# Kernel tuning notes

Hardware: AMD Instinct MI355X
Metric: run time of the kernel (lower is better)

## Reference

```python
import jax, jax.numpy as jnp
import numpy as np
from jax import lax

NUM_POINT = 2048   # S: number of FPS-sampled centers
RADIUS = 0.2       # ball-query radius
NUM_SAMPLE = 32    # K: neighbors per center


def setup_inputs() -> dict:
    key = jax.random.key(0)
    k1, k2 = jax.random.split(key)
    B, N, C = 4, 8192, 64
    xyz = jax.random.normal(k1, (B, N, 3), dtype=jnp.float32)
    features = jax.random.normal(k2, (B, C, N), dtype=jnp.float32)
    return {"xyz": xyz, "features": features}


def fps(xyz, npoint):
    """D-FPS (farthest point sampling on coords). xyz (B,N,3) -> idx (B,npoint) int32.
    Matches CUDA FPS: start at index 0, iteratively pick argmax of min-dist."""
    B, N, _ = xyz.shape

    def body(carry, _):
        min_d, last = carry
        p = jnp.take_along_axis(xyz, last[:, None, None], axis=1)  # (B,1,3)
        d = jnp.sum((xyz - p) ** 2, axis=-1)                        # (B,N)
        min_d = jnp.minimum(min_d, d)
        nxt = jnp.argmax(min_d, axis=-1).astype(jnp.int32)
        return (min_d, nxt), nxt

    idx0 = jnp.zeros((B,), jnp.int32)
    min_d0 = jnp.full((B, N), 1e10, dtype=xyz.dtype)
    (_, _), rest = lax.scan(body, (min_d0, idx0), None, length=npoint - 1)
    return jnp.concatenate([idx0[None], rest], axis=0).T  # (B, npoint)


def ball_query(radius, nsample, xyz, new_xyz):
    """For each center pick the first nsample point indices (in original order)
    with squared dist < radius^2; pad short lists with the first hit (0 if none).
    xyz (B,N,3), new_xyz (B,S,3) -> idx (B,S,nsample) int32."""
    N = xyz.shape[1]
    d2 = jnp.sum((new_xyz[:, :, None, :] - xyz[:, None, :, :]) ** 2, axis=-1)  # (B,S,N)
    mask = d2 < radius * radius
    # key = point index where in-ball, else N; nsample smallest keys = first hits in order
    key = jnp.where(mask, jnp.arange(N, dtype=jnp.int32)[None, None, :], N)
    _, idx = lax.top_k(-key, nsample)            # (B,S,nsample)
    idx = idx.astype(jnp.int32)
    valid = jnp.take_along_axis(mask, idx, axis=-1)
    first = jnp.where(valid[:, :, :1], idx[:, :, :1], 0)
    return jnp.where(valid, idx, first)


def reference(xyz, features):
    B, N, _ = xyz.shape
    C = features.shape[1]
    fps_idx = fps(xyz, NUM_POINT)                                       # (B,S)
    new_xyz = jnp.take_along_axis(xyz, fps_idx[:, :, None], axis=1)     # (B,S,3)
    idx = ball_query(RADIUS, NUM_SAMPLE, xyz, new_xyz)                  # (B,S,K)
    # grouped xyz, recentered on each sampled point
    grouped_xyz = jnp.take_along_axis(xyz[:, None], idx[..., None], axis=2)  # (B,S,K,3)
    grouped_xyz = grouped_xyz - new_xyz[:, :, None, :]
    # grouped features
    f = jnp.swapaxes(features, 1, 2)                                    # (B,N,C)
    grouped_f = jnp.take_along_axis(f[:, None], idx[..., None], axis=2)  # (B,S,K,C)
    # use_xyz=True: concat relative coords with features -> (B, 3+C, S, K)
    grouped = jnp.concatenate([grouped_xyz, grouped_f], axis=-1).transpose(0, 3, 1, 2)
    return (new_xyz, grouped, fps_idx)
```

## Files before the change

kernel.cpp:

```cpp
#include <hip/hip_runtime.h>

#define NPTS 8192
#define SPTS 2048
#define KS 32
#define CF 64
#define BQ 4
#define FPS_T 512
#define PPT (NPTS / FPS_T)
#define PPT2 (PPT / 2)
#define FPS_SHIFT 9

#define OFF_GROUPED 24576
#define GROUPED_SZ  17563648
#define OFF_FPSIDX  (OFF_GROUPED + GROUPED_SZ)

typedef __attribute__((ext_vector_type(2))) float vf2;
typedef unsigned long long u64;

#define DPPMAXF(x, ctrl) do {                                                   \
    int _t = __builtin_amdgcn_mov_dpp(__float_as_int(x), (ctrl), 0xf, 0xf, true); \
    x = fmaxf((x), __int_as_float(_t));                                         \
} while (0)

#define DPPMAXU(x, ctrl) do {                                                   \
    unsigned _u = (unsigned)__builtin_amdgcn_mov_dpp((int)(x), (ctrl), 0xf, 0xf, true); \
    x = ((x) > _u) ? (x) : _u;                                                  \
} while (0)

__global__ __launch_bounds__(FPS_T)
void fps_kernel(const float* __restrict__ xyz, float* __restrict__ out)
{
#pragma clang fp contract(off)
    __shared__ float sx[NPTS], sy[NPTS], sz[NPTS];
    __shared__ u64 slots[2][8];
    const int b    = blockIdx.x;
    const int tid  = threadIdx.x;
    const int wv   = tid >> 6;
    const int lane = tid & 63;
    const float* xb = xyz + (size_t)b * (NPTS * 3);

    vf2 PX[PPT2], PY[PPT2], PZ[PPT2], MD[PPT2];
#pragma unroll
    for (int j = 0; j < PPT2; ++j) {
        const int p0 = tid + FPS_T * (2 * j);
        const int p1 = p0 + FPS_T;
        const float x0 = xb[p0 * 3 + 0], y0 = xb[p0 * 3 + 1], z0 = xb[p0 * 3 + 2];
        const float x1 = xb[p1 * 3 + 0], y1 = xb[p1 * 3 + 1], z1 = xb[p1 * 3 + 2];
        sx[p0] = x0; sy[p0] = y0; sz[p0] = z0;
        sx[p1] = x1; sy[p1] = y1; sz[p1] = z1;
        vf2 vx; vx.x = x0; vx.y = x1; PX[j] = vx;
        vf2 vy; vy.x = y0; vy.y = y1; PY[j] = vy;
        vf2 vz; vz.x = z0; vz.y = z1; PZ[j] = vz;
        vf2 vm; vm.x = 1e10f; vm.y = 1e10f; MD[j] = vm;
    }

    float* newxyz = out;
    float* fpsidx = out + OFF_FPSIDX;

    float qx = xb[0], qy = xb[1], qz = xb[2];
    if (tid == 0) {
        fpsidx[(size_t)b * SPTS + 0] = 0.0f;
        newxyz[(size_t)b * SPTS * 3 + 0] = qx;
        newxyz[(size_t)b * SPTS * 3 + 1] = qy;
        newxyz[(size_t)b * SPTS * 3 + 2] = qz;
    }

    for (int i = 1; i < SPTS; ++i) {
        vf2 qxx; qxx.x = qx; qxx.y = qx;
        vf2 qyy; qyy.x = qy; qyy.y = qy;
        vf2 qzz; qzz.x = qz; qzz.y = qz;

#pragma unroll
        for (int j = 0; j < PPT2; ++j) {
            const vf2 dx = PX[j] - qxx;
            const vf2 dy = PY[j] - qyy;
            const vf2 dz = PZ[j] - qzz;
            const vf2 d  = (dx * dx + dy * dy) + dz * dz;
            MD[j] = __builtin_elementwise_min(MD[j], d);
        }

        vf2 m0 = __builtin_elementwise_max(MD[0], MD[1]);
        vf2 m1 = __builtin_elementwise_max(MD[2], MD[3]);
        vf2 m2 = __builtin_elementwise_max(MD[4], MD[5]);
        vf2 m3 = __builtin_elementwise_max(MD[6], MD[7]);
        m0 = __builtin_elementwise_max(m0, m1);
        m2 = __builtin_elementwise_max(m2, m3);
        m0 = __builtin_elementwise_max(m0, m2);
        const float best = fmaxf(m0.x, m0.y);

        int bj = PPT - 1;
#pragma unroll
        for (int j = PPT - 2; j >= 0; --j) {
            const float v = (j & 1) ? MD[j >> 1].y : MD[j >> 1].x;
            if (v == best) bj = j;
        }
        const int bidx = tid + (bj << FPS_SHIFT);

        float wm = best;
        DPPMAXF(wm, 0x111);
        DPPMAXF(wm, 0x112);
        DPPMAXF(wm, 0x114);
        DPPMAXF(wm, 0x118);
        DPPMAXF(wm, 0x142);
        DPPMAXF(wm, 0x143);
        const float wavemax =
            __int_as_float(__builtin_amdgcn_readlane(__float_as_int(wm), 63));

        unsigned cand = (best == wavemax) ? (unsigned)(NPTS - 1 - bidx) : 0u;
        DPPMAXU(cand, 0x111);
        DPPMAXU(cand, 0x112);
        DPPMAXU(cand, 0x114);
        DPPMAXU(cand, 0x118);
        DPPMAXU(cand, 0x142);
        DPPMAXU(cand, 0x143);
        const unsigned candmax =
            (unsigned)__builtin_amdgcn_readlane((int)cand, 63);

        const u64 pk = ((u64)__float_as_uint(wavemax) << 32) | candmax;
        if (lane == 0) slots[i & 1][wv] = pk;
        __syncthreads();

        u64 g = slots[i & 1][0];
#pragma unroll
        for (int w = 1; w < 8; ++w) {
            const u64 s = slots[i & 1][w];
            if (s > g) g = s;
        }
        const int widx = (NPTS - 1) - (int)(unsigned)(g & 0xffffffffull);

        qx = sx[widx]; qy = sy[widx]; qz = sz[widx];

        if (tid == 0) {
            fpsidx[(size_t)b * SPTS + i] = (float)widx;
            const size_t o = ((size_t)b * SPTS + i) * 3;
            newxyz[o + 0] = qx; newxyz[o + 1] = qy; newxyz[o + 2] = qz;
        }
    }
}

__global__ __launch_bounds__(256)
void ballgroup_kernel(const float* __restrict__ xyz, const float* __restrict__ feat,
                      float* out)
{
#pragma clang fp contract(off)
    __shared__ int idxl[4][KS];
    const int tid    = threadIdx.x;
    const int wv     = tid >> 6;
    const int lane   = tid & 63;
    const int center = blockIdx.x * 4 + wv;
    const int b      = center >> 11;
    const int s      = center & (SPTS - 1);
    const float* xb  = xyz + (size_t)b * (NPTS * 3);
    const float* newxyz = out;
    const float cx = newxyz[(size_t)center * 3 + 0];
    const float cy = newxyz[(size_t)center * 3 + 1];
    const float cz = newxyz[(size_t)center * 3 + 2];

    if (lane == 0) idxl[wv][0] = 0;

    int cnt = 0;
    for (int nb = 0; nb < NPTS; nb += 64) {
        const int p = nb + lane;
        const float x = xb[p * 3 + 0];
        const float y = xb[p * 3 + 1];
        const float z = xb[p * 3 + 2];
        const float dx = cx - x, dy = cy - y, dz = cz - z;
        const float d2 = (dx * dx + dy * dy) + dz * dz;
        const bool in = (d2 <= 0.04f);
        const unsigned long long mk = __ballot(in);
        if (in) {
            const int pos = cnt + __popcll(mk & ((1ull << lane) - 1ull));
            if (pos < KS) idxl[wv][pos] = p;
        }
        cnt += (int)__popcll(mk);
        if (cnt >= KS) break;
    }
    const int cc = cnt < KS ? cnt : KS;

    int myidx = 0;
    if (lane < KS) {
        myidx = (lane < cc) ? idxl[wv][lane] : idxl[wv][0];
        idxl[wv][lane] = myidx;
    }

    float* grouped = out + OFF_GROUPED;
    const size_t chstride = (size_t)SPTS * KS;
    const size_t base67   = (size_t)b * 67 * chstride + (size_t)s * KS;

    if (lane < KS) {
        const float gx = xb[(size_t)myidx * 3 + 0] - cx;
        const float gy = xb[(size_t)myidx * 3 + 1] - cy;
        const float gz = xb[(size_t)myidx * 3 + 2] - cz;
        grouped[base67 + 0 * chstride + lane] = gx;
        grouped[base67 + 1 * chstride + lane] = gy;
        grouped[base67 + 2 * chstride + lane] = gz;
    }

    const int k    = lane & (KS - 1);
    const int half = lane >> 5;
    const int gi   = idxl[wv][k];
    const float* fb = feat + (size_t)b * CF * NPTS;
    const size_t obase = base67 + 3 * chstride + (size_t)k;
#pragma unroll 8
    for (int c0 = 0; c0 < 32; ++c0) {
        const int c = c0 * 2 + half;
        grouped[obase + (size_t)c * chstride] = fb[(size_t)c * NPTS + gi];
    }
}

extern "C" void kernel_launch(void* const* d_in, const int* in_sizes, int n_in,
                              void* d_out, int out_size, void* d_ws, size_t ws_size,
                              hipStream_t stream) {
    const float* xyz  = (const float*)d_in[0];
    const float* feat = (const float*)d_in[1];
    float* out = (float*)d_out;
    fps_kernel<<<dim3(BQ), dim3(FPS_T), 0, stream>>>(xyz, out);
    ballgroup_kernel<<<dim3((BQ * SPTS) / 4), dim3(256), 0, stream>>>(xyz, feat, out);
}
```

Before: 1.907 ms.

## Fuse FPS wave argmax into single 64-bit DPP reduction and buffer results in LDS

The FPS loop now packs each lane's max distance and inverted index into one 64-bit key and reduces it with a single DPP chain. Before, it ran a float max reduction, a readlane, and then a second index reduction. The per-lane argmax scan is replaced by an equality bitmask plus count-trailing-zeros, and the cross-wave slot read uses 128-bit LDS loads. Per-iteration global stores of the sampled point and index are buffered in LDS and written out together after the loop. The goal is to shorten the serial critical path of each of the 2047 iterations, at the cost of more LDS use and 64-bit compares per DPP step.

```diff
diff --git a/kernel.cpp b/kernel.cpp
--- a/kernel.cpp
+++ b/kernel.cpp
@@ -17,14 +17,14 @@
 typedef __attribute__((ext_vector_type(2))) float vf2;
 typedef unsigned long long u64;
 
-#define DPPMAXF(x, ctrl) do {                                                   \
-    int _t = __builtin_amdgcn_mov_dpp(__float_as_int(x), (ctrl), 0xf, 0xf, true); \
-    x = fmaxf((x), __int_as_float(_t));                                         \
-} while (0)
-
-#define DPPMAXU(x, ctrl) do {                                                   \
-    unsigned _u = (unsigned)__builtin_amdgcn_mov_dpp((int)(x), (ctrl), 0xf, 0xf, true); \
-    x = ((x) > _u) ? (x) : _u;                                                  \
+#define DPPSTEP64(pk, ctrl) do {                                                  \
+    const unsigned _lo = (unsigned)(pk), _hi = (unsigned)((pk) >> 32);            \
+    const unsigned _olo =                                                         \
+        (unsigned)__builtin_amdgcn_mov_dpp((int)_lo, (ctrl), 0xf, 0xf, true);     \
+    const unsigned _ohi =                                                         \
+        (unsigned)__builtin_amdgcn_mov_dpp((int)_hi, (ctrl), 0xf, 0xf, true);     \
+    const u64 _o = ((u64)_ohi << 32) | _olo;                                      \
+    (pk) = (_o > (pk)) ? _o : (pk);                                               \
 } while (0)
 
 __global__ __launch_bounds__(FPS_T)
@@ -32,7 +32,8 @@
 {
 #pragma clang fp contract(off)
     __shared__ float sx[NPTS], sy[NPTS], sz[NPTS];
-    __shared__ u64 slots[2][8];
+    __shared__ float4 rres[SPTS];
+    __shared__ __align__(16) u64 slots[2][8];
     const int b    = blockIdx.x;
     const int tid  = threadIdx.x;
     const int wv   = tid >> 6;
@@ -54,15 +55,10 @@
         vf2 vm; vm.x = 1e10f; vm.y = 1e10f; MD[j] = vm;
     }
 
-    float* newxyz = out;
-    float* fpsidx = out + OFF_FPSIDX;
-
     float qx = xb[0], qy = xb[1], qz = xb[2];
     if (tid == 0) {
-        fpsidx[(size_t)b * SPTS + 0] = 0.0f;
-        newxyz[(size_t)b * SPTS * 3 + 0] = qx;
-        newxyz[(size_t)b * SPTS * 3 + 1] = qy;
-        newxyz[(size_t)b * SPTS * 3 + 2] = qz;
+        float4 r; r.x = qx; r.y = qy; r.z = qz; r.w = 0.0f;
+        rres[0] = r;
     }
 
     for (int i = 1; i < SPTS; ++i) {
@@ -88,53 +84,59 @@
         m0 = __builtin_elementwise_max(m0, m2);
         const float best = fmaxf(m0.x, m0.y);
 
-        int bj = PPT - 1;
+        unsigned k0 = ((MD[0].x == best) ? 0x0001u : 0u) | ((MD[0].y == best) ? 0x0002u : 0u);
+        unsigned k1 = ((MD[1].x == best) ? 0x0004u : 0u) | ((MD[1].y == best) ? 0x0008u : 0u);
+        unsigned k2 = ((MD[2].x == best) ? 0x0010u : 0u) | ((MD[2].y == best) ? 0x0020u : 0u);
+        unsigned k3 = ((MD[3].x == best) ? 0x0040u : 0u) | ((MD[3].y == best) ? 0x0080u : 0u);
+        unsigned k4 = ((MD[4].x == best) ? 0x0100u : 0u) | ((MD[4].y == best) ? 0x0200u : 0u);
+        unsigned k5 = ((MD[5].x == best) ? 0x0400u : 0u) | ((MD[5].y == best) ? 0x0800u : 0u);
+        unsigned k6 = ((MD[6].x == best) ? 0x1000u : 0u) | ((MD[6].y == best) ? 0x2000u : 0u);
+        unsigned k7 = ((MD[7].x == best) ? 0x4000u : 0u) | ((MD[7].y == best) ? 0x8000u : 0u);
+        k0 |= k1; k2 |= k3; k4 |= k5; k6 |= k7;
+        k0 |= k2; k4 |= k6;
+        const int bj = __builtin_ctz(k0 | k4);
+        const int bidx = tid + (bj << FPS_SHIFT);
+
+        u64 pk = ((u64)__float_as_uint(best) << 32) | (unsigned)(NPTS - 1 - bidx);
+
+        DPPSTEP64(pk, 0x111);
+        DPPSTEP64(pk, 0x112);
+        DPPSTEP64(pk, 0x114);
+        DPPSTEP64(pk, 0x118);
+        DPPSTEP64(pk, 0x142);
+        DPPSTEP64(pk, 0x143);
+        if (lane == 63) slots[i & 1][wv] = pk;
+        __syncthreads();
+
+        const ulonglong2* sp = (const ulonglong2*)slots[i & 1];
+        const ulonglong2 p0 = sp[0], p1 = sp[1], p2 = sp[2], p3 = sp[3];
+        u64 a = p0.x > p0.y ? p0.x : p0.y;
+        u64 c = p1.x > p1.y ? p1.x : p1.y;
+        u64 d = p2.x > p2.y ? p2.x : p2.y;
+        u64 e = p3.x > p3.y ? p3.x : p3.y;
+        a = a > c ? a : c;
+        d = d > e ? d : e;
+        const u64 g = a > d ? a : d;
+        const int widx = (NPTS - 1) - (int)(unsigned)(g & 0xffffffffull);
+
+        qx = sx[widx]; qy = sy[widx]; qz = sz[widx];
+
+        if (tid == 0) {
+            float4 r; r.x = qx; r.y = qy; r.z = qz; r.w = (float)widx;
+            rres[i] = r;
+        }
+    }
+
+    __syncthreads();
+    float* newxyz = out;
+    float* fpsidx = out + OFF_FPSIDX;
 #pragma unroll
-        for (int j = PPT - 2; j >= 0; --j) {
-            const float v = (j & 1) ? MD[j >> 1].y : MD[j >> 1].x;
-            if (v == best) bj = j;
-        }
-        const int bidx = tid + (bj << FPS_SHIFT);
-
-        float wm = best;
-        DPPMAXF(wm, 0x111);
-        DPPMAXF(wm, 0x112);
-        DPPMAXF(wm, 0x114);
-        DPPMAXF(wm, 0x118);
-        DPPMAXF(wm, 0x142);
-        DPPMAXF(wm, 0x143);
-        const float wavemax =
-            __int_as_float(__builtin_amdgcn_readlane(__float_as_int(wm), 63));
-
-        unsigned cand = (best == wavemax) ? (unsigned)(NPTS - 1 - bidx) : 0u;
-        DPPMAXU(cand, 0x111);
-        DPPMAXU(cand, 0x112);
-        DPPMAXU(cand, 0x114);
-        DPPMAXU(cand, 0x118);
-        DPPMAXU(cand, 0x142);
-        DPPMAXU(cand, 0x143);
-        const unsigned candmax =
-            (unsigned)__builtin_amdgcn_readlane((int)cand, 63);
-
-        const u64 pk = ((u64)__float_as_uint(wavemax) << 32) | candmax;
-        if (lane == 0) slots[i & 1][wv] = pk;
-        __syncthreads();
-
-        u64 g = slots[i & 1][0];
-#pragma unroll
-        for (int w = 1; w < 8; ++w) {
-            const u64 s = slots[i & 1][w];
-            if (s > g) g = s;
-        }
-        const int widx = (NPTS - 1) - (int)(unsigned)(g & 0xffffffffull);
-
-        qx = sx[widx]; qy = sy[widx]; qz = sz[widx];
-
-        if (tid == 0) {
-            fpsidx[(size_t)b * SPTS + i] = (float)widx;
-            const size_t o = ((size_t)b * SPTS + i) * 3;
-            newxyz[o + 0] = qx; newxyz[o + 1] = qy; newxyz[o + 2] = qz;
-        }
+    for (int j = 0; j < 4; ++j) {
+        const int i = tid + (j << FPS_SHIFT);
+        const float4 r = rres[i];
+        fpsidx[(size_t)b * SPTS + i] = r.w;
+        const size_t o = ((size_t)b * SPTS + i) * 3;
+        newxyz[o + 0] = r.x; newxyz[o + 1] = r.y; newxyz[o + 2] = r.z;
     }
 }
 
```

After: 2.051 ms. +7.6%, slower.

## Halve FPS block size, buffer results in LDS, and streamline argmax reduction

Applied to the files above, without the earlier changes.

The FPS kernel now runs 256 threads with 32 points per thread instead of 512 with 16. This cuts the barrier to 4 waves and the cross-wave slot reduction to two 16-byte LDS reads. Per-iteration global stores of sampled indices and coordinates are buffered in an LDS array and written out cooperatively at the end. Other changes: the argmax index search uses a bitmask plus ctz, the separate readlane of the candidate is dropped by having lane 63 write the slot, and inline packed add/mul asm keeps the arithmetic unfused. More work per thread raises register pressure and per-iteration serial ALU work, in exchange for cheaper synchronisation.

```diff
diff --git a/kernel.cpp b/kernel.cpp
--- a/kernel.cpp
+++ b/kernel.cpp
@@ -5,10 +5,10 @@
 #define KS 32
 #define CF 64
 #define BQ 4
-#define FPS_T 512
-#define PPT (NPTS / FPS_T)
-#define PPT2 (PPT / 2)
-#define FPS_SHIFT 9
+#define FPS_T 256
+#define PPT 32
+#define NPAIR 16
+#define FPS_SHIFT 8
 
 #define OFF_GROUPED 24576
 #define GROUPED_SZ  17563648
@@ -16,6 +16,13 @@
 
 typedef __attribute__((ext_vector_type(2))) float vf2;
 typedef unsigned long long u64;
+
+static __device__ __forceinline__ vf2 pk_add(vf2 a, vf2 b) {
+    vf2 d; asm("v_pk_add_f32 %0, %1, %2" : "=v"(d) : "v"(a), "v"(b)); return d;
+}
+static __device__ __forceinline__ vf2 pk_mul(vf2 a, vf2 b) {
+    vf2 d; asm("v_pk_mul_f32 %0, %1, %2" : "=v"(d) : "v"(a), "v"(b)); return d;
+}
 
 #define DPPMAXF(x, ctrl) do {                                                   \
     int _t = __builtin_amdgcn_mov_dpp(__float_as_int(x), (ctrl), 0xf, 0xf, true); \
@@ -32,18 +39,19 @@
 {
 #pragma clang fp contract(off)
     __shared__ float sx[NPTS], sy[NPTS], sz[NPTS];
-    __shared__ u64 slots[2][8];
+    __shared__ float4 rres[SPTS];
+    __shared__ __align__(16) u64 slots[2][4];
     const int b    = blockIdx.x;
     const int tid  = threadIdx.x;
     const int wv   = tid >> 6;
     const int lane = tid & 63;
     const float* xb = xyz + (size_t)b * (NPTS * 3);
 
-    vf2 PX[PPT2], PY[PPT2], PZ[PPT2], MD[PPT2];
-#pragma unroll
-    for (int j = 0; j < PPT2; ++j) {
-        const int p0 = tid + FPS_T * (2 * j);
-        const int p1 = p0 + FPS_T;
+    vf2 PX[NPAIR], PY[NPAIR], PZ[NPAIR], MD[NPAIR];
+#pragma unroll
+    for (int j = 0; j < NPAIR; ++j) {
+        const int p0 = tid + 512 * j;
+        const int p1 = p0 + 256;
         const float x0 = xb[p0 * 3 + 0], y0 = xb[p0 * 3 + 1], z0 = xb[p0 * 3 + 2];
         const float x1 = xb[p1 * 3 + 0], y1 = xb[p1 * 3 + 1], z1 = xb[p1 * 3 + 2];
         sx[p0] = x0; sy[p0] = y0; sz[p0] = z0;
@@ -54,47 +62,46 @@
         vf2 vm; vm.x = 1e10f; vm.y = 1e10f; MD[j] = vm;
     }
 
-    float* newxyz = out;
-    float* fpsidx = out + OFF_FPSIDX;
-
     float qx = xb[0], qy = xb[1], qz = xb[2];
     if (tid == 0) {
-        fpsidx[(size_t)b * SPTS + 0] = 0.0f;
-        newxyz[(size_t)b * SPTS * 3 + 0] = qx;
-        newxyz[(size_t)b * SPTS * 3 + 1] = qy;
-        newxyz[(size_t)b * SPTS * 3 + 2] = qz;
+        float4 r; r.x = qx; r.y = qy; r.z = qz; r.w = 0.0f;
+        rres[0] = r;
     }
 
     for (int i = 1; i < SPTS; ++i) {
-        vf2 qxx; qxx.x = qx; qxx.y = qx;
-        vf2 qyy; qyy.x = qy; qyy.y = qy;
-        vf2 qzz; qzz.x = qz; qzz.y = qz;
-
-#pragma unroll
-        for (int j = 0; j < PPT2; ++j) {
-            const vf2 dx = PX[j] - qxx;
-            const vf2 dy = PY[j] - qyy;
-            const vf2 dz = PZ[j] - qzz;
-            const vf2 d  = (dx * dx + dy * dy) + dz * dz;
-            MD[j] = __builtin_elementwise_min(MD[j], d);
-        }
-
-        vf2 m0 = __builtin_elementwise_max(MD[0], MD[1]);
-        vf2 m1 = __builtin_elementwise_max(MD[2], MD[3]);
-        vf2 m2 = __builtin_elementwise_max(MD[4], MD[5]);
-        vf2 m3 = __builtin_elementwise_max(MD[6], MD[7]);
-        m0 = __builtin_elementwise_max(m0, m1);
-        m2 = __builtin_elementwise_max(m2, m3);
-        m0 = __builtin_elementwise_max(m0, m2);
-        const float best = fmaxf(m0.x, m0.y);
-
-        int bj = PPT - 1;
-#pragma unroll
-        for (int j = PPT - 2; j >= 0; --j) {
-            const float v = (j & 1) ? MD[j >> 1].y : MD[j >> 1].x;
-            if (v == best) bj = j;
-        }
-        const int bidx = tid + (bj << FPS_SHIFT);
+        const float nqx = -qx, nqy = -qy, nqz = -qz;
+        vf2 vnx; vnx.x = nqx; vnx.y = nqx;
+        vf2 vny; vny.x = nqy; vny.y = nqy;
+        vf2 vnz; vnz.x = nqz; vnz.y = nqz;
+
+#pragma unroll
+        for (int j = 0; j < NPAIR; ++j) {
+            const vf2 dx = pk_add(PX[j], vnx);
+            const vf2 dy = pk_add(PY[j], vny);
+            const vf2 dz = pk_add(PZ[j], vnz);
+            const vf2 xx = pk_mul(dx, dx);
+            const vf2 yy = pk_mul(dy, dy);
+            const vf2 zz = pk_mul(dz, dz);
+            const vf2 s  = pk_add(pk_add(xx, yy), zz);
+            MD[j] = __builtin_elementwise_min(MD[j], s);
+        }
+
+        vf2 t0 = __builtin_elementwise_max(MD[0],  MD[1]);
+        vf2 t1 = __builtin_elementwise_max(MD[2],  MD[3]);
+        vf2 t2 = __builtin_elementwise_max(MD[4],  MD[5]);
+        vf2 t3 = __builtin_elementwise_max(MD[6],  MD[7]);
+        vf2 t4 = __builtin_elementwise_max(MD[8],  MD[9]);
+        vf2 t5 = __builtin_elementwise_max(MD[10], MD[11]);
+        vf2 t6 = __builtin_elementwise_max(MD[12], MD[13]);
+        vf2 t7 = __builtin_elementwise_max(MD[14], MD[15]);
+        t0 = __builtin_elementwise_max(t0, t1);
+        t2 = __builtin_elementwise_max(t2, t3);
+        t4 = __builtin_elementwise_max(t4, t5);
+        t6 = __builtin_elementwise_max(t6, t7);
+        t0 = __builtin_elementwise_max(t0, t2);
+        t4 = __builtin_elementwise_max(t4, t6);
+        t0 = __builtin_elementwise_max(t0, t4);
+        const float best = fmaxf(t0.x, t0.y);
 
         float wm = best;
         DPPMAXF(wm, 0x111);
@@ -106,6 +113,15 @@
         const float wavemax =
             __int_as_float(__builtin_amdgcn_readlane(__float_as_int(wm), 63));
 
+        unsigned m = 0u;
+#pragma unroll
+        for (int j = 0; j < NPAIR; ++j) {
+            m |= (MD[j].x == best) ? (1u << (2 * j))     : 0u;
+            m |= (MD[j].y == best) ? (1u << (2 * j + 1)) : 0u;
+        }
+        const int bo = __builtin_ctz(m);
+        const int bidx = tid + (bo << FPS_SHIFT);
+
         unsigned cand = (best == wavemax) ? (unsigned)(NPTS - 1 - bidx) : 0u;
         DPPMAXU(cand, 0x111);
         DPPMAXU(cand, 0x112);
@@ -113,28 +129,36 @@
         DPPMAXU(cand, 0x118);
         DPPMAXU(cand, 0x142);
         DPPMAXU(cand, 0x143);
-        const unsigned candmax =
-            (unsigned)__builtin_amdgcn_readlane((int)cand, 63);
-
-        const u64 pk = ((u64)__float_as_uint(wavemax) << 32) | candmax;
-        if (lane == 0) slots[i & 1][wv] = pk;
+
+        if (lane == 63)
+            slots[i & 1][wv] = ((u64)__float_as_uint(wm) << 32) | cand;
         __syncthreads();
 
-        u64 g = slots[i & 1][0];
-#pragma unroll
-        for (int w = 1; w < 8; ++w) {
-            const u64 s = slots[i & 1][w];
-            if (s > g) g = s;
-        }
-        const int widx = (NPTS - 1) - (int)(unsigned)(g & 0xffffffffull);
+        const ulonglong2* sp = (const ulonglong2*)slots[i & 1];
+        const ulonglong2 pA = sp[0], pB = sp[1];
+        u64 a = pA.x > pA.y ? pA.x : pA.y;
+        u64 c = pB.x > pB.y ? pB.x : pB.y;
+        const u64 g = a > c ? a : c;
+        const int widx = (NPTS - 1) - (int)(unsigned)g;
 
         qx = sx[widx]; qy = sy[widx]; qz = sz[widx];
 
         if (tid == 0) {
-            fpsidx[(size_t)b * SPTS + i] = (float)widx;
-            const size_t o = ((size_t)b * SPTS + i) * 3;
-            newxyz[o + 0] = qx; newxyz[o + 1] = qy; newxyz[o + 2] = qz;
-        }
+            float4 r; r.x = qx; r.y = qy; r.z = qz; r.w = (float)widx;
+            rres[i] = r;
+        }
+    }
+
+    __syncthreads();
+    float* newxyz = out;
+    float* fpsidx = out + OFF_FPSIDX;
+#pragma unroll
+    for (int j = 0; j < 8; ++j) {
+        const int i = tid + (j << FPS_SHIFT);
+        const float4 r = rres[i];
+        fpsidx[(size_t)b * SPTS + i] = r.w;
+        const size_t o = ((size_t)b * SPTS + i) * 3;
+        newxyz[o + 0] = r.x; newxyz[o + 1] = r.y; newxyz[o + 2] = r.z;
     }
 }
 
```

After: 2.104 ms. +10.3%, slower.

## Broadcast FPS winner coords via LDS slots and defer global writes

Applied to the files above, without the earlier changes.

Removes the full LDS copy of the point cloud and instead has the winning lane of each wave publish its coordinates next to its key. After the barrier, the selected coordinates are pulled with readlane, which shortens the serial dependency chain of each iteration. The wave reduction replaces the row-crossing DPP steps with four readlanes and scalar max. Per-iteration global writes are buffered in LDS and flushed once at the end. This adds more register work in the per-iteration selection loop.

```diff
diff --git a/kernel.cpp b/kernel.cpp
--- a/kernel.cpp
+++ b/kernel.cpp
@@ -6,8 +6,8 @@
 #define CF 64
 #define BQ 4
 #define FPS_T 512
-#define PPT (NPTS / FPS_T)
-#define PPT2 (PPT / 2)
+#define PPT 16
+#define NPAIR 8
 #define FPS_SHIFT 9
 
 #define OFF_GROUPED 24576
@@ -27,51 +27,48 @@
     x = ((x) > _u) ? (x) : _u;                                                  \
 } while (0)
 
+static __device__ __forceinline__ unsigned umax2(unsigned a, unsigned b) {
+    return a > b ? a : b;
+}
+
 __global__ __launch_bounds__(FPS_T)
 void fps_kernel(const float* __restrict__ xyz, float* __restrict__ out)
 {
 #pragma clang fp contract(off)
-    __shared__ float sx[NPTS], sy[NPTS], sz[NPTS];
-    __shared__ u64 slots[2][8];
+    __shared__ float4 rres[SPTS];
+    __shared__ __align__(16) u64 slotA[2][8];
+    __shared__ __align__(16) float slotB[2][32];
     const int b    = blockIdx.x;
     const int tid  = threadIdx.x;
     const int wv   = tid >> 6;
     const int lane = tid & 63;
     const float* xb = xyz + (size_t)b * (NPTS * 3);
 
-    vf2 PX[PPT2], PY[PPT2], PZ[PPT2], MD[PPT2];
-#pragma unroll
-    for (int j = 0; j < PPT2; ++j) {
-        const int p0 = tid + FPS_T * (2 * j);
-        const int p1 = p0 + FPS_T;
-        const float x0 = xb[p0 * 3 + 0], y0 = xb[p0 * 3 + 1], z0 = xb[p0 * 3 + 2];
-        const float x1 = xb[p1 * 3 + 0], y1 = xb[p1 * 3 + 1], z1 = xb[p1 * 3 + 2];
-        sx[p0] = x0; sy[p0] = y0; sz[p0] = z0;
-        sx[p1] = x1; sy[p1] = y1; sz[p1] = z1;
-        vf2 vx; vx.x = x0; vx.y = x1; PX[j] = vx;
-        vf2 vy; vy.x = y0; vy.y = y1; PY[j] = vy;
-        vf2 vz; vz.x = z0; vz.y = z1; PZ[j] = vz;
+    vf2 PX[NPAIR], PY[NPAIR], PZ[NPAIR], MD[NPAIR];
+#pragma unroll
+    for (int j = 0; j < NPAIR; ++j) {
+        const int p0 = tid + 1024 * j;
+        const int p1 = p0 + 512;
+        vf2 vx; vx.x = xb[p0 * 3 + 0]; vx.y = xb[p1 * 3 + 0]; PX[j] = vx;
+        vf2 vy; vy.x = xb[p0 * 3 + 1]; vy.y = xb[p1 * 3 + 1]; PY[j] = vy;
+        vf2 vz; vz.x = xb[p0 * 3 + 2]; vz.y = xb[p1 * 3 + 2]; PZ[j] = vz;
         vf2 vm; vm.x = 1e10f; vm.y = 1e10f; MD[j] = vm;
     }
-
-    float* newxyz = out;
-    float* fpsidx = out + OFF_FPSIDX;
 
     float qx = xb[0], qy = xb[1], qz = xb[2];
     if (tid == 0) {
-        fpsidx[(size_t)b * SPTS + 0] = 0.0f;
-        newxyz[(size_t)b * SPTS * 3 + 0] = qx;
-        newxyz[(size_t)b * SPTS * 3 + 1] = qy;
-        newxyz[(size_t)b * SPTS * 3 + 2] = qz;
+        float4 r; r.x = qx; r.y = qy; r.z = qz; r.w = 0.0f;
+        rres[0] = r;
     }
 
     for (int i = 1; i < SPTS; ++i) {
+        const int par = i & 1;
         vf2 qxx; qxx.x = qx; qxx.y = qx;
         vf2 qyy; qyy.x = qy; qyy.y = qy;
         vf2 qzz; qzz.x = qz; qzz.y = qz;
 
 #pragma unroll
-        for (int j = 0; j < PPT2; ++j) {
+        for (int j = 0; j < NPAIR; ++j) {
             const vf2 dx = PX[j] - qxx;
             const vf2 dy = PY[j] - qyy;
             const vf2 dz = PZ[j] - qzz;
@@ -79,62 +76,93 @@
             MD[j] = __builtin_elementwise_min(MD[j], d);
         }
 
-        vf2 m0 = __builtin_elementwise_max(MD[0], MD[1]);
-        vf2 m1 = __builtin_elementwise_max(MD[2], MD[3]);
-        vf2 m2 = __builtin_elementwise_max(MD[4], MD[5]);
-        vf2 m3 = __builtin_elementwise_max(MD[6], MD[7]);
-        m0 = __builtin_elementwise_max(m0, m1);
-        m2 = __builtin_elementwise_max(m2, m3);
-        m0 = __builtin_elementwise_max(m0, m2);
-        const float best = fmaxf(m0.x, m0.y);
-
-        int bj = PPT - 1;
-#pragma unroll
-        for (int j = PPT - 2; j >= 0; --j) {
-            const float v = (j & 1) ? MD[j >> 1].y : MD[j >> 1].x;
-            if (v == best) bj = j;
-        }
-        const int bidx = tid + (bj << FPS_SHIFT);
+        vf2 t0 = __builtin_elementwise_max(MD[0], MD[1]);
+        vf2 t1 = __builtin_elementwise_max(MD[2], MD[3]);
+        vf2 t2 = __builtin_elementwise_max(MD[4], MD[5]);
+        vf2 t3 = __builtin_elementwise_max(MD[6], MD[7]);
+        t0 = __builtin_elementwise_max(t0, t1);
+        t2 = __builtin_elementwise_max(t2, t3);
+        t0 = __builtin_elementwise_max(t0, t2);
+        const float best = fmaxf(t0.x, t0.y);
+        const unsigned bbits = __float_as_uint(best);
 
         float wm = best;
         DPPMAXF(wm, 0x111);
         DPPMAXF(wm, 0x112);
         DPPMAXF(wm, 0x114);
         DPPMAXF(wm, 0x118);
-        DPPMAXF(wm, 0x142);
-        DPPMAXF(wm, 0x143);
-        const float wavemax =
-            __int_as_float(__builtin_amdgcn_readlane(__float_as_int(wm), 63));
-
-        unsigned cand = (best == wavemax) ? (unsigned)(NPTS - 1 - bidx) : 0u;
+        const unsigned f0 = (unsigned)__builtin_amdgcn_readlane(__float_as_int(wm), 15);
+        const unsigned f1 = (unsigned)__builtin_amdgcn_readlane(__float_as_int(wm), 31);
+        const unsigned f2 = (unsigned)__builtin_amdgcn_readlane(__float_as_int(wm), 47);
+        const unsigned f3 = (unsigned)__builtin_amdgcn_readlane(__float_as_int(wm), 63);
+        const unsigned wavemaxbits = umax2(umax2(f0, f1), umax2(f2, f3));
+
+        int bo = PPT - 1;
+        float xw = PX[NPAIR - 1].y, yw = PY[NPAIR - 1].y, zw = PZ[NPAIR - 1].y;
+#pragma unroll
+        for (int j = PPT - 2; j >= 0; --j) {
+            const float mdv = (j & 1) ? MD[j >> 1].y : MD[j >> 1].x;
+            if (mdv == best) {
+                bo = j;
+                xw = (j & 1) ? PX[j >> 1].y : PX[j >> 1].x;
+                yw = (j & 1) ? PY[j >> 1].y : PY[j >> 1].x;
+                zw = (j & 1) ? PZ[j >> 1].y : PZ[j >> 1].x;
+            }
+        }
+        const unsigned negbidx = (unsigned)(NPTS - 1 - (tid + (bo << FPS_SHIFT)));
+
+        unsigned cand = (bbits == wavemaxbits) ? negbidx : 0u;
         DPPMAXU(cand, 0x111);
         DPPMAXU(cand, 0x112);
         DPPMAXU(cand, 0x114);
         DPPMAXU(cand, 0x118);
-        DPPMAXU(cand, 0x142);
-        DPPMAXU(cand, 0x143);
-        const unsigned candmax =
-            (unsigned)__builtin_amdgcn_readlane((int)cand, 63);
-
-        const u64 pk = ((u64)__float_as_uint(wavemax) << 32) | candmax;
-        if (lane == 0) slots[i & 1][wv] = pk;
+        const unsigned c0 = (unsigned)__builtin_amdgcn_readlane((int)cand, 15);
+        const unsigned c1 = (unsigned)__builtin_amdgcn_readlane((int)cand, 31);
+        const unsigned c2 = (unsigned)__builtin_amdgcn_readlane((int)cand, 47);
+        const unsigned c3 = (unsigned)__builtin_amdgcn_readlane((int)cand, 63);
+        const unsigned candmax = umax2(umax2(c0, c1), umax2(c2, c3));
+
+        if (bbits == wavemaxbits && negbidx == candmax) {
+            slotA[par][wv] = ((u64)wavemaxbits << 32) | candmax;
+            float4 sb; sb.x = xw; sb.y = yw; sb.z = zw; sb.w = 0.0f;
+            *(float4*)&slotB[par][wv * 4] = sb;
+        }
         __syncthreads();
 
-        u64 g = slots[i & 1][0];
-#pragma unroll
-        for (int w = 1; w < 8; ++w) {
-            const u64 s = slots[i & 1][w];
-            if (s > g) g = s;
-        }
+        const float vB = slotB[par][lane & 31];
+        const ulonglong2* sp = (const ulonglong2*)slotA[par];
+        const ulonglong2 pA = sp[0], pB = sp[1], pC = sp[2], pD = sp[3];
+        u64 a = pA.x > pA.y ? pA.x : pA.y;
+        u64 c = pB.x > pB.y ? pB.x : pB.y;
+        u64 d = pC.x > pC.y ? pC.x : pC.y;
+        u64 e = pD.x > pD.y ? pD.x : pD.y;
+        a = a > c ? a : c;
+        d = d > e ? d : e;
+        const u64 g = a > d ? a : d;
         const int widx = (NPTS - 1) - (int)(unsigned)(g & 0xffffffffull);
 
-        qx = sx[widx]; qy = sy[widx]; qz = sz[widx];
+        const int wstar = (widx >> 6) & 7;
+        const int sw = __builtin_amdgcn_readfirstlane(wstar) * 4;
+        qx = __int_as_float(__builtin_amdgcn_readlane(__float_as_int(vB), sw + 0));
+        qy = __int_as_float(__builtin_amdgcn_readlane(__float_as_int(vB), sw + 1));
+        qz = __int_as_float(__builtin_amdgcn_readlane(__float_as_int(vB), sw + 2));
 
         if (tid == 0) {
-            fpsidx[(size_t)b * SPTS + i] = (float)widx;
-            const size_t o = ((size_t)b * SPTS + i) * 3;
-            newxyz[o + 0] = qx; newxyz[o + 1] = qy; newxyz[o + 2] = qz;
-        }
+            float4 r; r.x = qx; r.y = qy; r.z = qz; r.w = (float)widx;
+            rres[i] = r;
+        }
+    }
+
+    __syncthreads();
+    float* newxyz = out;
+    float* fpsidx = out + OFF_FPSIDX;
+#pragma unroll
+    for (int j = 0; j < 4; ++j) {
+        const int i = tid + (j << FPS_SHIFT);
+        const float4 r = rres[i];
+        fpsidx[(size_t)b * SPTS + i] = r.w;
+        const size_t o = ((size_t)b * SPTS + i) * 3;
+        newxyz[o + 0] = r.x; newxyz[o + 1] = r.y; newxyz[o + 2] = r.z;
     }
 }
 
```

Measured after the change: 2.422 ms. +27.0%, slower.
